# Optimization experiments

Measured on AMD Instinct MI355X. Metric: run time of the kernel, lower is better.

## Reference

```python
import jax, jax.numpy as jnp
import numpy as np

# ---- static config (from MACEConfig / MACELayerConfig) ----
N_NODES = 128
F_S = 128          # n_invariant_feat_hidden (0e channels)
F_V = 64           # n_vectors_hidden (1e channels)
N_BESSEL = 8       # bessel_number
R_MAX = 5.0        # r_max
N_LAYERS = 2       # n_interactions
HID_RAD = 64       # radial MLP hidden width
F_S_OUT = 128      # n_invariant_feat_readout
F_V_OUT = 64       # n_vectors_readout
AVG_NEIGH = float(N_NODES)  # avg_num_neighbors default = n_nodes
RAD_OUT = F_S + 3 * F_V     # per-edge radial channel weights for the 4 TP paths


def _senders_receivers(n):
    # fully connected graph, matching get_senders_and_receivers
    s = np.repeat(np.arange(n), n - 1)
    j = np.tile(np.arange(1, n), n)
    r = (s + j) % n
    return jnp.asarray(s, dtype=jnp.int32), jnp.asarray(r, dtype=jnp.int32)


def _bessel(r):
    # e3nn bessel basis: sqrt(2/c) sin(n pi r / c) / r, n = 1..N_BESSEL
    n = jnp.arange(1, N_BESSEL + 1, dtype=r.dtype)
    return jnp.sqrt(2.0 / R_MAX) * jnp.sin(n * jnp.pi * r[:, None] / R_MAX) / r[:, None]


def _envelope(r):
    # smooth radial cutoff (polynomial p=6), stand-in for e3nn soft_envelope
    u = r / R_MAX
    p = 6.0
    env = 1.0 - (p + 1) * (p + 2) / 2 * u ** p + p * (p + 2) * u ** (p + 1) - p * (p + 1) / 2 * u ** (p + 2)
    return jnp.where(u < 1.0, env, 0.0)


def _forward(x, species_embed, Wr1, Wr2, W_sv, W_mix_s, W_mix_v, W_out_s, W_out_v):
    senders, receivers = _senders_receivers(N_NODES)

    def single(pos):  # pos: (N, 3)
        com = pos.mean(axis=0)                       # centre of mass (3,)
        v = pos[receivers] - pos[senders]            # edge relative vectors (E, 3)
        r = jnp.linalg.norm(v, axis=-1) + 1e-8       # (E,)
        vhat = v / r[:, None]
        rb = _bessel(r) * _envelope(r)[:, None]      # (E, N_BESSEL)

        s = jnp.broadcast_to(species_embed[0], (N_NODES, F_S))       # 0e node feats
        V = jnp.zeros((N_NODES, F_V, 3), dtype=pos.dtype)            # 1e node feats

        for l in range(N_LAYERS):
            # learned per-edge radial weights for each tensor-product path
            h = jax.nn.silu(rb @ Wr1[l]) @ Wr2[l]    # (E, RAD_OUT)
            R0 = h[:, :F_S]
            R1 = h[:, F_S:F_S + F_V]
            R2 = h[:, F_S + F_V:F_S + 2 * F_V]
            R3 = h[:, F_S + 2 * F_V:]

            s_src = s[senders]                       # gather (E, F_S)
            V_src = V[senders]                       # gather (E, F_V, 3)

            # CG tensor-product paths (only 0e and 1e irreps present):
            m0a = R0 * s_src                                         # 0e x 0e -> 0e
            m0b = R1 * jnp.einsum('efk,ek->ef', V_src, vhat)         # 1e x 1e -> 0e
            m1a = (R2 * (s_src @ W_sv[l]))[..., None] * vhat[:, None, :]  # 0e x 1e -> 1e
            m1b = R3[..., None] * V_src                              # 1e x 0e -> 1e

            # scatter-sum message passing over receivers
            agg0 = jax.ops.segment_sum(jnp.concatenate([m0a, m0b], -1), receivers,
                                       num_segments=N_NODES) / AVG_NEIGH   # (N, F_S+F_V)
            agg1 = jax.ops.segment_sum(jnp.concatenate([m1a, m1b], 1), receivers,
                                       num_segments=N_NODES) / AVG_NEIGH   # (N, 2F_V, 3)

            s = s + jax.nn.silu(agg0 @ W_mix_s[l])
            V = V + jnp.einsum('nfk,fg->ngk', agg1, W_mix_v[l])

        out_s = s @ W_out_s                                          # (N, F_S_OUT)
        out_v = jnp.einsum('nfk,fg->ngk', V, W_out_v) + com          # (N, F_V_OUT, 3) + CoM
        return out_v, out_s

    return jax.vmap(single)(x)


def setup_inputs() -> dict:
    key = jax.random.key(0)
    ks = jax.random.split(key, 10)
    sc = lambda fan: 1.0 / np.sqrt(fan)
    inp = {
        'x': jax.random.normal(ks[0], (8, N_NODES, 3), dtype=jnp.float32),
        'species_embed': jax.random.normal(ks[1], (1, F_S), dtype=jnp.float32),
        'Wr1': jax.random.normal(ks[2], (N_LAYERS, N_BESSEL, HID_RAD), dtype=jnp.float32) * sc(N_BESSEL),
        'Wr2': jax.random.normal(ks[3], (N_LAYERS, HID_RAD, RAD_OUT), dtype=jnp.float32) * sc(HID_RAD),
        'W_sv': jax.random.normal(ks[4], (N_LAYERS, F_S, F_V), dtype=jnp.float32) * sc(F_S),
        'W_mix_s': jax.random.normal(ks[5], (N_LAYERS, F_S + F_V, F_S), dtype=jnp.float32) * sc(F_S + F_V),
        'W_mix_v': jax.random.normal(ks[6], (N_LAYERS, 2 * F_V, F_V), dtype=jnp.float32) * sc(2 * F_V),
        'W_out_s': jax.random.normal(ks[7], (F_S, F_S_OUT), dtype=jnp.float32) * sc(F_S),
        'W_out_v': jax.random.normal(ks[8], (F_V, F_V_OUT), dtype=jnp.float32) * sc(F_V),
    }
    return inp


def reference(x, species_embed, Wr1, Wr2, W_sv, W_mix_s, W_mix_v, W_out_s, W_out_v):
    return _forward(x, species_embed, Wr1, Wr2, W_sv, W_mix_s, W_mix_v, W_out_s, W_out_v)
```

## Files before the change

### kernel.cpp

```cpp
#include <hip/hip_runtime.h>
#include <math.h>

typedef unsigned short u16;
typedef __attribute__((ext_vector_type(8))) short frag_ab;
typedef __attribute__((ext_vector_type(4))) float frag_cd;

#define BATCH 8
#define NN 128
#define FS 128
#define FV 64
#define NB 8
#define HID 64
#define ROUT 320
#define HSTRB 72

#define SZ_S (BATCH*FS*NN)
#define SZ_V (BATCH*FV*3*NN)
#define SZ_T (BATCH*FV*NN)
#define N_W2B (ROUT*HID)
#define OFF_SB 0
#define OFF_VB (OFF_SB+SZ_S)
#define OFF_T1 (OFF_VB+SZ_V)
#define OFF_W2B (OFF_T1+SZ_T)

__device__ __forceinline__ float silu_f(float x){ return x * (1.0f/(1.0f + __expf(-x))); }

__device__ __forceinline__ u16 f2bf(float x){
  union { float f; unsigned int u; } v; v.f = x;
  unsigned int r = v.u + 0x7fffu + ((v.u >> 16) & 1u);
  return (u16)(r >> 16);
}
__device__ __forceinline__ float bf2f(u16 h){
  union { unsigned int u; float f; } v; v.u = ((unsigned int)h) << 16; return v.f;
}

__global__ __launch_bounds__(512) void layer0_kernel(
    const float* __restrict__ pos,
    const float* __restrict__ species,
    const float* __restrict__ Wr1l,
    const float* __restrict__ Wr2,
    const float* __restrict__ Wsv,
    const float* __restrict__ WmixSl,
    const float* __restrict__ WmixVl,
    float* __restrict__ sOut,
    float* __restrict__ vOut,
    float* __restrict__ tOut,
    u16*   __restrict__ w2b)
{
  const int tid = threadIdx.x;
  const int b   = blockIdx.x >> 6;
  const int k0  = (blockIdx.x & 63) * 2;

  __shared__ u16   hidB[2][128*HSTRB];
  __shared__ float vhx[2][128], vhy[2][128], vhz[2][128];
  __shared__ float colsum[2][4][64];
  __shared__ float aggS[2][128];
  __shared__ float dV[2][192];
  __shared__ float sNew[2][128];
  __shared__ float t0L[64];

  const float* pb   = pos + b*NN*3;
  const float* Wr2l = Wr2;

  {
    const int kk   = tid >> 8;
    const int r2   = tid & 255;
    const int i    = r2 & 127;
    const int half = r2 >> 7;
    const int k    = k0 + kk;
    float vx = pb[k*3+0]-pb[i*3+0];
    float vy = pb[k*3+1]-pb[i*3+1];
    float vz = pb[k*3+2]-pb[i*3+2];
    float r = sqrtf(vx*vx+vy*vy+vz*vz) + 1e-8f;
    float inv = 1.0f/r;
    if (half==0){ vhx[kk][i]=vx*inv; vhy[kk][i]=vy*inv; vhz[kk][i]=vz*inv; }
    float u = r*0.2f;
    float env = 0.0f;
    if (u < 1.0f && i != k){
      float u2=u*u, u6=u2*u2*u2;
      env = 1.0f - 28.0f*u6 + 48.0f*u6*u - 21.0f*u6*u2;
    }
    float coef = 0.6324555320336759f * inv * env;
    float th   = r * 0.6283185307179586f;
    float s1 = __sinf(th), c1 = __cosf(th);
    float rb[NB];
    rb[0] = coef*s1;
    float twoc = 2.f*c1, sp = s1, spp = 0.f;
    #pragma unroll
    for(int n=1;n<NB;n++){ float s = twoc*sp - spp; spp = sp; sp = s; rb[n] = coef*s; }
    u16* hrow = hidB[kk] + i*HSTRB;
    #pragma unroll
    for(int jg=0;jg<8;jg++){
      const int jgg = half*8 + jg;
      float h0=0.f,h1=0.f,h2=0.f,h3=0.f;
      #pragma unroll
      for(int n=0;n<NB;n++){
        const float* wr = Wr1l + n*HID + jgg*4;
        float rn = rb[n];
        h0 = fmaf(rn, wr[0], h0);
        h1 = fmaf(rn, wr[1], h1);
        h2 = fmaf(rn, wr[2], h2);
        h3 = fmaf(rn, wr[3], h3);
      }
      ushort4 uu = make_ushort4(f2bf(silu_f(h0)), f2bf(silu_f(h1)),
                                f2bf(silu_f(h2)), f2bf(silu_f(h3)));
      *(ushort4*)(hrow + jgg*4) = uu;
    }
  }
  __syncthreads();

  {
    const int kk  = tid >> 8;
    const int var = (tid >> 6) & 3;
    const int j   = tid & 63;
    const u16* hb = hidB[kk];
    float a0 = 0.f, a1 = 0.f;
    if (var == 0){
      #pragma unroll 8
      for (int i=0;i<128;i+=2){
        a0 += bf2f(hb[i*HSTRB + j]);
        a1 += bf2f(hb[(i+1)*HSTRB + j]);
      }
    } else {
      const float* wv = (var==1) ? vhx[kk] : (var==2) ? vhy[kk] : vhz[kk];
      #pragma unroll 8
      for (int i=0;i<128;i+=2){
        a0 = fmaf(bf2f(hb[i*HSTRB + j]),     wv[i],   a0);
        a1 = fmaf(bf2f(hb[(i+1)*HSTRB + j]), wv[i+1], a1);
      }
    }
    colsum[kk][var][j] = a0+a1;
  }
  __syncthreads();

  if (tid < 128){
    const int c = tid;
    float d00=0.f,d01=0.f, d10=0.f,d11=0.f;
    #pragma unroll 8
    for (int j=0;j<HID;j+=2){
      float w0 = Wr2l[j*ROUT + c];
      float w1 = Wr2l[(j+1)*ROUT + c];
      d00 = fmaf(colsum[0][0][j],   w0, d00);
      d01 = fmaf(colsum[0][0][j+1], w1, d01);
      d10 = fmaf(colsum[1][0][j],   w0, d10);
      d11 = fmaf(colsum[1][0][j+1], w1, d11);
    }
    float sc = species[c] * (1.0f/128.0f);
    aggS[0][c] = sc * (d00+d01);
    aggS[1][c] = sc * (d10+d11);
  } else if (tid < 320){
    const int o = tid - 128;
    const int f = o & 63, c3 = o >> 6;
    float d00=0.f,d01=0.f, d10=0.f,d11=0.f;
    #pragma unroll 8
    for (int j=0;j<HID;j+=2){
      float w0 = Wr2l[j*ROUT + 192 + f];
      float w1 = Wr2l[(j+1)*ROUT + 192 + f];
      d00 = fmaf(colsum[0][1+c3][j],   w0, d00);
      d01 = fmaf(colsum[0][1+c3][j+1], w1, d01);
      d10 = fmaf(colsum[1][1+c3][j],   w0, d10);
      d11 = fmaf(colsum[1][1+c3][j+1], w1, d11);
    }
    dV[0][f*3+c3] = (d00+d01) * (1.0f/128.0f);
    dV[1][f*3+c3] = (d10+d11) * (1.0f/128.0f);
  } else if (tid < 384){
    const int g = tid - 320;
    float a0=0.f, a1=0.f;
    #pragma unroll 8
    for (int c=0; c<FS; c+=2){
      a0 = fmaf(species[c],   Wsv[c*FV+g],     a0);
      a1 = fmaf(species[c+1], Wsv[(c+1)*FV+g], a1);
    }
    t0L[g] = a0+a1;
  } else if (tid < 424){
    const int t = blockIdx.x*40 + (tid-384);
    const int j = t & 63, c = t >> 6;
    w2b[t] = f2bf(Wr2[HID*ROUT + j*ROUT + c]);
  }
  __syncthreads();

  if (tid < FS){
    float a00=0.f,a01=0.f, a10=0.f,a11=0.f;
    #pragma unroll 8
    for (int cc=0; cc<128; cc+=2){
      float w0 = WmixSl[cc*FS+tid];
      float w1 = WmixSl[(cc+1)*FS+tid];
      a00 = fmaf(aggS[0][cc],   w0, a00);
      a01 = fmaf(aggS[0][cc+1], w1, a01);
      a10 = fmaf(aggS[1][cc],   w0, a10);
      a11 = fmaf(aggS[1][cc+1], w1, a11);
    }
    float sn0 = species[tid] + silu_f(a00+a01);
    float sn1 = species[tid] + silu_f(a10+a11);
    sNew[0][tid] = sn0;
    sNew[1][tid] = sn1;
    sOut[(b*FS+tid)*NN + k0]     = sn0;
    sOut[(b*FS+tid)*NN + k0 + 1] = sn1;
  } else if (tid < 320){
    const int o = tid - 128;
    const int g = o/3, c3 = o - g*3;
    float a0=0.f, a1=0.f;
    #pragma unroll 8
    for (int f=0; f<FV; f++){
      float w = WmixVl[f*FV+g];
      float tf = t0L[f];
      a0 = fmaf(tf*dV[0][f*3+c3], w, a0);
      a1 = fmaf(tf*dV[1][f*3+c3], w, a1);
    }
    vOut[(b*FV*3 + o)*NN + k0]     = a0;
    vOut[(b*FV*3 + o)*NN + k0 + 1] = a1;
  }
  __syncthreads();

  if (tid < FV){
    const float* Wsv1 = Wsv + FS*FV;
    float a00=0.f,a01=0.f, a10=0.f,a11=0.f;
    #pragma unroll 8
    for (int f=0; f<FS; f+=2){
      float w0 = Wsv1[f*FV+tid];
      float w1 = Wsv1[(f+1)*FV+tid];
      a00 = fmaf(sNew[0][f],   w0, a00);
      a01 = fmaf(sNew[0][f+1], w1, a01);
      a10 = fmaf(sNew[1][f],   w0, a10);
      a11 = fmaf(sNew[1][f+1], w1, a11);
    }
    tOut[(b*FV+tid)*NN + k0]     = (a00+a01);
    tOut[(b*FV+tid)*NN + k0 + 1] = (a10+a11);
  }
}

__global__ __launch_bounds__(1024) void layer_kernel(
    const float* __restrict__ pos,
    const float* __restrict__ sIn,
    const float* __restrict__ vIn,
    const float* __restrict__ tIn,
    const float* __restrict__ Wr1l,
    const u16*   __restrict__ w2bl,
    const float* __restrict__ WmixSl,
    const float* __restrict__ WmixVl,
    const float* __restrict__ WoutS,
    const float* __restrict__ WoutV,
    float* __restrict__ outp)
{
  const int tid  = threadIdx.x;
  const int b    = blockIdx.x >> 5;
  const int k0   = (blockIdx.x & 31) * 4;
  const int w    = tid >> 6;
  const int lane = tid & 63;
  const int col  = lane & 15;
  const int quad = lane >> 4;
  const int gh   = w & 1;
  const int wq   = (w >> 1) & 3;
  const int sh   = w >> 3;

  __shared__ u16   hidB[4][128*HSTRB];
  __shared__ float vhx[4][128], vhy[4][128], vhz[4][128];
  __shared__ float aggP[4][2][576];
  __shared__ float sPart[4][4][FS];
  __shared__ float sNew[4][FS];
  __shared__ float vNewL[4][192];
  __shared__ float comL[3];

  const float* pb = pos + b*NN*3;

  {
    const int jh = tid >> 9;
    const int kk = (tid >> 7) & 3;
    const int i  = tid & 127;
    const int k  = k0 + kk;
    float vx = pb[k*3+0]-pb[i*3+0];
    float vy = pb[k*3+1]-pb[i*3+1];
    float vz = pb[k*3+2]-pb[i*3+2];
    float r = sqrtf(vx*vx+vy*vy+vz*vz) + 1e-8f;
    float inv = 1.0f/r;
    if (jh == 0){ vhx[kk][i]=vx*inv; vhy[kk][i]=vy*inv; vhz[kk][i]=vz*inv; }
    float u = r*0.2f;
    float env = 0.0f;
    if (u < 1.0f && i != k){
      float u2=u*u, u6=u2*u2*u2;
      env = 1.0f - 28.0f*u6 + 48.0f*u6*u - 21.0f*u6*u2;
    }
    float coef = 0.6324555320336759f * inv * env;
    float th   = r * 0.6283185307179586f;
    float s1 = __sinf(th), c1 = __cosf(th);
    float rb[NB];
    rb[0] = coef*s1;
    float twoc = 2.f*c1, sp = s1, spp = 0.f;
    #pragma unroll
    for(int n=1;n<NB;n++){ float s = twoc*sp - spp; spp = sp; sp = s; rb[n] = coef*s; }
    u16* hrow = hidB[kk] + i*HSTRB;
    #pragma unroll
    for(int jg0=0;jg0<8;jg0++){
      const int jg = jh*8 + jg0;
      float h0=0.f,h1=0.f,h2=0.f,h3=0.f;
      #pragma unroll
      for(int n=0;n<NB;n++){
        const float* wr = Wr1l + n*HID + jg*4;
        float rn = rb[n];
        h0 = fmaf(rn, wr[0], h0);
        h1 = fmaf(rn, wr[1], h1);
        h2 = fmaf(rn, wr[2], h2);
        h3 = fmaf(rn, wr[3], h3);
      }
      ushort4 uu = make_ushort4(f2bf(silu_f(h0)), f2bf(silu_f(h1)),
                                f2bf(silu_f(h2)), f2bf(silu_f(h3)));
      *(ushort4*)(hrow + jg*4) = uu;
    }
    if (tid < 3){
      float a0=0.f, a1=0.f;
      for (int n=0;n<NN;n+=2){ a0 += pb[n*3+tid]; a1 += pb[(n+1)*3+tid]; }
      comL[tid] = (a0+a1) * (1.0f/128.0f);
    }
  }
  __syncthreads();

  const float* sIb = sIn + b*FS*NN;
  const float* vIb = vIn + b*FV*3*NN;
  const float* tIb = tIn + b*FV*NN;
  const int i00 = sh*64 + quad*4;

  if (gh == 0){
    const int c_s0 = wq*16 + col;
    const int c_s1 = 64 + c_s0;

    const u16* wp0 = w2bl + c_s0*HID + quad*8;
    const u16* wp1 = w2bl + c_s1*HID + quad*8;
    const u16* wp2 = w2bl + (128 + c_s0)*HID + quad*8;
    const frag_ab b00 = *(const frag_ab*)(wp0), b01 = *(const frag_ab*)(wp0+32);
    const frag_ab b10 = *(const frag_ab*)(wp1), b11 = *(const frag_ab*)(wp1+32);
    const frag_ab b20 = *(const frag_ab*)(wp2), b21 = *(const frag_ab*)(wp2+32);

    const float* fs0 = sIb + c_s0*NN + i00;
    const float* fs1 = sIb + c_s1*NN + i00;
    const float* fv  = vIb + c_s0*3*NN + i00;

    float sA0[4]={0.f,0.f,0.f,0.f}, sA1[4]={0.f,0.f,0.f,0.f}, sA2[4]={0.f,0.f,0.f,0.f};

    #pragma unroll 1
    for (int mt=0; mt<4; mt++){
      float4 s4a = *(const float4*)&fs0[mt*16];
      float4 s4b = *(const float4*)&fs1[mt*16];
      float4 vx4 = *(const float4*)&fv[mt*16];
      float4 vy4 = *(const float4*)&fv[NN + mt*16];
      float4 vz4 = *(const float4*)&fv[2*NN + mt*16];
      const int hbase = (sh*64 + mt*16 + col)*HSTRB + quad*8;
      const int vbase = i00 + mt*16;
      #pragma unroll
      for (int kk=0; kk<4; kk++){
        frag_ab a0 = *(const frag_ab*)&hidB[kk][hbase];
        frag_ab a1 = *(const frag_ab*)&hidB[kk][hbase + 32];
        float4 hx4 = *(const float4*)&vhx[kk][vbase];
        float4 hy4 = *(const float4*)&vhy[kk][vbase];
        float4 hz4 = *(const float4*)&vhz[kk][vbase];
        frag_cd ac0 = {0.f,0.f,0.f,0.f};
        frag_cd ac1 = {0.f,0.f,0.f,0.f};
        frag_cd ac2 = {0.f,0.f,0.f,0.f};
        ac0 = __builtin_amdgcn_mfma_f32_16x16x32_bf16(a0, b00, ac0, 0,0,0);
        ac1 = __builtin_amdgcn_mfma_f32_16x16x32_bf16(a0, b10, ac1, 0,0,0);
        ac2 = __builtin_amdgcn_mfma_f32_16x16x32_bf16(a0, b20, ac2, 0,0,0);
        ac0 = __builtin_amdgcn_mfma_f32_16x16x32_bf16(a1, b01, ac0, 0,0,0);
        ac1 = __builtin_amdgcn_mfma_f32_16x16x32_bf16(a1, b11, ac1, 0,0,0);
        ac2 = __builtin_amdgcn_mfma_f32_16x16x32_bf16(a1, b21, ac2, 0,0,0);

        sA0[kk] += ac0[0]*s4a.x + ac0[1]*s4a.y + ac0[2]*s4a.z + ac0[3]*s4a.w;
        sA1[kk] += ac1[0]*s4b.x + ac1[1]*s4b.y + ac1[2]*s4b.z + ac1[3]*s4b.w;
        sA2[kk] += ac2[0]*(vx4.x*hx4.x + vy4.x*hy4.x + vz4.x*hz4.x)
                 + ac2[1]*(vx4.y*hx4.y + vy4.y*hy4.y + vz4.y*hz4.y)
                 + ac2[2]*(vx4.z*hx4.z + vy4.z*hy4.z + vz4.z*hz4.z)
                 + ac2[3]*(vx4.w*hx4.w + vy4.w*hy4.w + vz4.w*hz4.w);
      }
    }
    #pragma unroll
    for (int kk=0; kk<4; kk++){
      float v0 = sA0[kk]; v0 += __shfl_xor(v0,16,64); v0 += __shfl_xor(v0,32,64);
      float v1 = sA1[kk]; v1 += __shfl_xor(v1,16,64); v1 += __shfl_xor(v1,32,64);
      float v2 = sA2[kk]; v2 += __shfl_xor(v2,16,64); v2 += __shfl_xor(v2,32,64);
      if (lane < 16){
        aggP[kk][sh][wq*16 + lane]       = v0;
        aggP[kk][sh][64 + wq*16 + lane]  = v1;
        aggP[kk][sh][128 + wq*16 + lane] = v2;
      }
    }
  } else {
    const int f_vc = wq*16 + col;

    const u16* wp3 = w2bl + (192 + f_vc)*HID + quad*8;
    const u16* wp4 = w2bl + (256 + f_vc)*HID + quad*8;
    const frag_ab b30 = *(const frag_ab*)(wp3), b31 = *(const frag_ab*)(wp3+32);
    const frag_ab b40 = *(const frag_ab*)(wp4), b41 = *(const frag_ab*)(wp4+32);

    const float* fv = vIb + f_vc*3*NN + i00;
    const float* ft = tIb + f_vc*NN + i00;

    float sX3[4]={0.f,0.f,0.f,0.f}, sY3[4]={0.f,0.f,0.f,0.f}, sZ3[4]={0.f,0.f,0.f,0.f};
    float sX4[4]={0.f,0.f,0.f,0.f}, sY4[4]={0.f,0.f,0.f,0.f}, sZ4[4]={0.f,0.f,0.f,0.f};

    #pragma unroll 1
    for (int mt=0; mt<4; mt++){
      float4 vx4 = *(const float4*)&fv[mt*16];
      float4 vy4 = *(const float4*)&fv[NN + mt*16];
      float4 vz4 = *(const float4*)&fv[2*NN + mt*16];
      float4 t4  = *(const float4*)&ft[mt*16];
      const int hbase = (sh*64 + mt*16 + col)*HSTRB + quad*8;
      const int vbase = i00 + mt*16;
      #pragma unroll
      for (int kk=0; kk<4; kk++){
        frag_ab a0 = *(const frag_ab*)&hidB[kk][hbase];
        frag_ab a1 = *(const frag_ab*)&hidB[kk][hbase + 32];
        float4 hx4 = *(const float4*)&vhx[kk][vbase];
        float4 hy4 = *(const float4*)&vhy[kk][vbase];
        float4 hz4 = *(const float4*)&vhz[kk][vbase];
        frag_cd ac3 = {0.f,0.f,0.f,0.f};
        frag_cd ac4 = {0.f,0.f,0.f,0.f};
        ac3 = __builtin_amdgcn_mfma_f32_16x16x32_bf16(a0, b30, ac3, 0,0,0);
        ac4 = __builtin_amdgcn_mfma_f32_16x16x32_bf16(a0, b40, ac4, 0,0,0);
        ac3 = __builtin_amdgcn_mfma_f32_16x16x32_bf16(a1, b31, ac3, 0,0,0);
        ac4 = __builtin_amdgcn_mfma_f32_16x16x32_bf16(a1, b41, ac4, 0,0,0);

        float t0_ = ac3[0]*t4.x, t1_ = ac3[1]*t4.y, t2_ = ac3[2]*t4.z, t3_ = ac3[3]*t4.w;
        sX3[kk] += t0_*hx4.x + t1_*hx4.y + t2_*hx4.z + t3_*hx4.w;
        sY3[kk] += t0_*hy4.x + t1_*hy4.y + t2_*hy4.z + t3_*hy4.w;
        sZ3[kk] += t0_*hz4.x + t1_*hz4.y + t2_*hz4.z + t3_*hz4.w;
        sX4[kk] += ac4[0]*vx4.x + ac4[1]*vx4.y + ac4[2]*vx4.z + ac4[3]*vx4.w;
        sY4[kk] += ac4[0]*vy4.x + ac4[1]*vy4.y + ac4[2]*vy4.z + ac4[3]*vy4.w;
        sZ4[kk] += ac4[0]*vz4.x + ac4[1]*vz4.y + ac4[2]*vz4.z + ac4[3]*vz4.w;
      }
    }
    #pragma unroll
    for (int kk=0; kk<4; kk++){
      float x3 = sX3[kk]; x3 += __shfl_xor(x3,16,64); x3 += __shfl_xor(x3,32,64);
      float y3 = sY3[kk]; y3 += __shfl_xor(y3,16,64); y3 += __shfl_xor(y3,32,64);
      float z3 = sZ3[kk]; z3 += __shfl_xor(z3,16,64); z3 += __shfl_xor(z3,32,64);
      float x4 = sX4[kk]; x4 += __shfl_xor(x4,16,64); x4 += __shfl_xor(x4,32,64);
      float y4 = sY4[kk]; y4 += __shfl_xor(y4,16,64); y4 += __shfl_xor(y4,32,64);
      float z4 = sZ4[kk]; z4 += __shfl_xor(z4,16,64); z4 += __shfl_xor(z4,32,64);
      if (lane < 16){
        const int f2 = wq*16 + lane;
        aggP[kk][sh][192+f2*3+0] = x3; aggP[kk][sh][192+f2*3+1] = y3; aggP[kk][sh][192+f2*3+2] = z3;
        aggP[kk][sh][384+f2*3+0] = x4; aggP[kk][sh][384+f2*3+1] = y4; aggP[kk][sh][384+f2*3+2] = z4;
      }
    }
  }

  __syncthreads();
  for (int t2=tid; t2<2304; t2+=1024){
    const int kk = t2 / 576;
    const int t  = t2 - kk*576;
    aggP[kk][0][t] = (aggP[kk][0][t] + aggP[kk][1][t]) * (1.0f/128.0f);
  }
  __syncthreads();

  if (tid < 512){
    const int o = tid & 127, p = tid >> 7;
    const int c0 = p*48;
    float a0=0.f,a1=0.f,a2=0.f,a3=0.f;
    #pragma unroll 8
    for (int cc=c0; cc<c0+48; cc++){
      float w0 = WmixSl[cc*FS+o];
      a0 = fmaf(aggP[0][0][cc], w0, a0);
      a1 = fmaf(aggP[1][0][cc], w0, a1);
      a2 = fmaf(aggP[2][0][cc], w0, a2);
      a3 = fmaf(aggP[3][0][cc], w0, a3);
    }
    sPart[0][p][o] = a0; sPart[1][p][o] = a1;
    sPart[2][p][o] = a2; sPart[3][p][o] = a3;
  } else if (tid < 704){
    const int o = tid - 512;
    const int g = o/3, c3 = o - g*3;
    float a0=0.f,a1=0.f,a2=0.f,a3=0.f;
    #pragma unroll 8
    for (int f=0; f<FV; f++){
      float w0 = WmixVl[f*FV+g];
      float w1 = WmixVl[(f+FV)*FV+g];
      a0 = fmaf(aggP[0][0][192+f*3+c3], w0, a0); a0 = fmaf(aggP[0][0][384+f*3+c3], w1, a0);
      a1 = fmaf(aggP[1][0][192+f*3+c3], w0, a1); a1 = fmaf(aggP[1][0][384+f*3+c3], w1, a1);
      a2 = fmaf(aggP[2][0][192+f*3+c3], w0, a2); a2 = fmaf(aggP[2][0][384+f*3+c3], w1, a2);
      a3 = fmaf(aggP[3][0][192+f*3+c3], w0, a3); a3 = fmaf(aggP[3][0][384+f*3+c3], w1, a3);
    }
    vNewL[0][o] = vIb[o*NN + k0]     + a0;
    vNewL[1][o] = vIb[o*NN + k0 + 1] + a1;
    vNewL[2][o] = vIb[o*NN + k0 + 2] + a2;
    vNewL[3][o] = vIb[o*NN + k0 + 3] + a3;
  }
  __syncthreads();

  if (tid < FS){
    #pragma unroll
    for (int kk=0; kk<4; kk++)
      sNew[kk][tid] = sIb[tid*NN + k0 + kk]
                    + silu_f(sPart[kk][0][tid] + sPart[kk][1][tid]
                           + sPart[kk][2][tid] + sPart[kk][3][tid]);
  } else if (tid < 320){
    const int o = tid - 128;
    const int g = o/3, c3 = o - g*3;
    float a0 = comL[c3], a1 = comL[c3], a2 = comL[c3], a3 = comL[c3];
    #pragma unroll 8
    for (int f=0; f<FV; f++){
      float wv = WoutV[f*FV+g];
      a0 = fmaf(vNewL[0][f*3+c3], wv, a0);
      a1 = fmaf(vNewL[1][f*3+c3], wv, a1);
      a2 = fmaf(vNewL[2][f*3+c3], wv, a2);
      a3 = fmaf(vNewL[3][f*3+c3], wv, a3);
    }
    outp[(b*NN+k0)*FV*3 + o]   = a0;
    outp[(b*NN+k0+1)*FV*3 + o] = a1;
    outp[(b*NN+k0+2)*FV*3 + o] = a2;
    outp[(b*NN+k0+3)*FV*3 + o] = a3;
  }
  __syncthreads();

  float* e3s = &aggP[0][0][0];
  if (tid < 512){
    const int o = tid & 127, p = tid >> 7;
    const int f0 = p*32;
    float a0=0.f,a1=0.f,a2=0.f,a3=0.f;
    #pragma unroll 8
    for (int f=f0; f<f0+32; f++){
      float w0 = WoutS[f*FS+o];
      a0 = fmaf(sNew[0][f], w0, a0);
      a1 = fmaf(sNew[1][f], w0, a1);
      a2 = fmaf(sNew[2][f], w0, a2);
      a3 = fmaf(sNew[3][f], w0, a3);
    }
    e3s[(p*4+0)*128 + o] = a0;
    e3s[(p*4+1)*128 + o] = a1;
    e3s[(p*4+2)*128 + o] = a2;
    e3s[(p*4+3)*128 + o] = a3;
  }
  __syncthreads();

  if (tid < 512){
    const int o = tid & 127, kk = tid >> 7;
    float a = e3s[(0*4+kk)*128 + o] + e3s[(1*4+kk)*128 + o]
            + e3s[(2*4+kk)*128 + o] + e3s[(3*4+kk)*128 + o];
    outp[BATCH*NN*FV*3 + (b*NN+k0+kk)*FS + o] = a;
  }
}

extern "C" void kernel_launch(void* const* d_in, const int* in_sizes, int n_in,
                              void* d_out, int out_size, void* d_ws, size_t ws_size,
                              hipStream_t stream)
{
  const float* x       = (const float*)d_in[0];
  const float* species = (const float*)d_in[1];
  const float* Wr1     = (const float*)d_in[2];
  const float* Wr2     = (const float*)d_in[3];
  const float* Wsv     = (const float*)d_in[4];
  const float* WmixS   = (const float*)d_in[5];
  const float* WmixV   = (const float*)d_in[6];
  const float* WoutS   = (const float*)d_in[7];
  const float* WoutV   = (const float*)d_in[8];
  float* ws  = (float*)d_ws;
  float* out = (float*)d_out;

  float* sB  = ws + OFF_SB;
  float* vB  = ws + OFF_VB;
  float* t1  = ws + OFF_T1;
  u16*   w2b = (u16*)(ws + OFF_W2B);

  layer0_kernel<<<BATCH*NN/2, 512, 0, stream>>>(x, species, Wr1, Wr2, Wsv,
      WmixS, WmixV, sB, vB, t1, w2b);

  layer_kernel<<<BATCH*NN/4, 1024, 0, stream>>>(x, sB, vB, t1,
      Wr1 + NB*HID, w2b, WmixS + 192*FS, WmixV + 128*FV,
      WoutS, WoutV, out);
}
```

Measured before the change: 126.0 us.

## Vectorise shared-memory reads with padded channel-major layouts and split t-projection

Rewrites the small per-node matvec loops in both kernels to read shared-memory operands as float4 instead of scalars. The vector aggregates dV, aggP and vNewL move from interleaved xyz to padded channel-major rows so those float4 reads are possible. The colsum reduction now loads two bf16 values per 32-bit read on half the threads, and the first kernel's t-projection is split across four thread groups with a shared-memory reduction. This cuts LDS instruction count and serial FMA depth, at the cost of an extra barrier and slightly more shared memory.

```diff
diff --git a/kernel.cpp b/kernel.cpp
--- a/kernel.cpp
+++ b/kernel.cpp
@@ -55,9 +55,10 @@
   __shared__ float vhx[2][128], vhy[2][128], vhz[2][128];
   __shared__ float colsum[2][4][64];
   __shared__ float aggS[2][128];
-  __shared__ float dV[2][192];
+  __shared__ float dV[2][204];
   __shared__ float sNew[2][128];
   __shared__ float t0L[64];
+  __shared__ float tPart[4][2][64];
 
   const float* pb   = pos + b*NN*3;
   const float* Wr2l = Wr2;
@@ -109,60 +110,72 @@
   }
   __syncthreads();
 
-  {
-    const int kk  = tid >> 8;
-    const int var = (tid >> 6) & 3;
-    const int j   = tid & 63;
-    const u16* hb = hidB[kk];
-    float a0 = 0.f, a1 = 0.f;
+  if (tid < 256){
+    const int kk = tid >> 7;
+    const int var = (tid >> 5) & 3;
+    const int jh  = tid & 31;
+    const u16* hb = hidB[kk] + 2*jh;
+    float a0=0.f,a1=0.f,c0_=0.f,c1_=0.f;
     if (var == 0){
       #pragma unroll 8
       for (int i=0;i<128;i+=2){
-        a0 += bf2f(hb[i*HSTRB + j]);
-        a1 += bf2f(hb[(i+1)*HSTRB + j]);
+        unsigned int v0 = *(const unsigned int*)(hb + i*HSTRB);
+        unsigned int v1 = *(const unsigned int*)(hb + (i+1)*HSTRB);
+        a0  += bf2f((u16)(v0 & 0xffffu)); a1  += bf2f((u16)(v0 >> 16));
+        c0_ += bf2f((u16)(v1 & 0xffffu)); c1_ += bf2f((u16)(v1 >> 16));
       }
     } else {
       const float* wv = (var==1) ? vhx[kk] : (var==2) ? vhy[kk] : vhz[kk];
       #pragma unroll 8
       for (int i=0;i<128;i+=2){
-        a0 = fmaf(bf2f(hb[i*HSTRB + j]),     wv[i],   a0);
-        a1 = fmaf(bf2f(hb[(i+1)*HSTRB + j]), wv[i+1], a1);
-      }
-    }
-    colsum[kk][var][j] = a0+a1;
+        unsigned int v0 = *(const unsigned int*)(hb + i*HSTRB);
+        unsigned int v1 = *(const unsigned int*)(hb + (i+1)*HSTRB);
+        float w0 = wv[i], w1 = wv[i+1];
+        a0  = fmaf(bf2f((u16)(v0 & 0xffffu)), w0, a0);
+        a1  = fmaf(bf2f((u16)(v0 >> 16)),     w0, a1);
+        c0_ = fmaf(bf2f((u16)(v1 & 0xffffu)), w1, c0_);
+        c1_ = fmaf(bf2f((u16)(v1 >> 16)),     w1, c1_);
+      }
+    }
+    colsum[kk][var][2*jh]   = a0+c0_;
+    colsum[kk][var][2*jh+1] = a1+c1_;
   }
   __syncthreads();
 
   if (tid < 128){
     const int c = tid;
-    float d00=0.f,d01=0.f, d10=0.f,d11=0.f;
-    #pragma unroll 8
-    for (int j=0;j<HID;j+=2){
-      float w0 = Wr2l[j*ROUT + c];
-      float w1 = Wr2l[(j+1)*ROUT + c];
-      d00 = fmaf(colsum[0][0][j],   w0, d00);
-      d01 = fmaf(colsum[0][0][j+1], w1, d01);
-      d10 = fmaf(colsum[1][0][j],   w0, d10);
-      d11 = fmaf(colsum[1][0][j+1], w1, d11);
+    float d0=0.f, d1=0.f;
+    #pragma unroll 2
+    for (int j0=0;j0<HID;j0+=4){
+      float4 s0 = *(const float4*)&colsum[0][0][j0];
+      float4 s1 = *(const float4*)&colsum[1][0][j0];
+      float w0 = Wr2l[j0*ROUT + c];
+      float w1 = Wr2l[(j0+1)*ROUT + c];
+      float w2 = Wr2l[(j0+2)*ROUT + c];
+      float w3 = Wr2l[(j0+3)*ROUT + c];
+      d0 = fmaf(s0.x,w0,d0); d0 = fmaf(s0.y,w1,d0); d0 = fmaf(s0.z,w2,d0); d0 = fmaf(s0.w,w3,d0);
+      d1 = fmaf(s1.x,w0,d1); d1 = fmaf(s1.y,w1,d1); d1 = fmaf(s1.z,w2,d1); d1 = fmaf(s1.w,w3,d1);
     }
     float sc = species[c] * (1.0f/128.0f);
-    aggS[0][c] = sc * (d00+d01);
-    aggS[1][c] = sc * (d10+d11);
+    aggS[0][c] = sc * d0;
+    aggS[1][c] = sc * d1;
   } else if (tid < 320){
     const int o = tid - 128;
     const int f = o & 63, c3 = o >> 6;
-    float d00=0.f,d01=0.f, d10=0.f,d11=0.f;
-    #pragma unroll 8
-    for (int j=0;j<HID;j+=2){
-      float w0 = Wr2l[j*ROUT + 192 + f];
-      float w1 = Wr2l[(j+1)*ROUT + 192 + f];
-      d00 = fmaf(colsum[0][1+c3][j],   w0, d00);
-      d01 = fmaf(colsum[0][1+c3][j+1], w1, d01);
-      d10 = fmaf(colsum[1][1+c3][j],   w0, d10);
-      d11 = fmaf(colsum[1][1+c3][j+1], w1, d11);
-    }
-    dV[0][f*3+c3] = (d00+d01) * (1.0f/128.0f);
-    dV[1][f*3+c3] = (d10+d11) * (1.0f/128.0f);
+    float d0=0.f, d1=0.f;
+    #pragma unroll 2
+    for (int j0=0;j0<HID;j0+=4){
+      float4 s0 = *(const float4*)&colsum[0][1+c3][j0];
+      float4 s1 = *(const float4*)&colsum[1][1+c3][j0];
+      float w0 = Wr2l[j0*ROUT + 192 + f];
+      float w1 = Wr2l[(j0+1)*ROUT + 192 + f];
+      float w2 = Wr2l[(j0+2)*ROUT + 192 + f];
+      float w3 = Wr2l[(j0+3)*ROUT + 192 + f];
+      d0 = fmaf(s0.x,w0,d0); d0 = fmaf(s0.y,w1,d0); d0 = fmaf(s0.z,w2,d0); d0 = fmaf(s0.w,w3,d0);
+      d1 = fmaf(s1.x,w0,d1); d1 = fmaf(s1.y,w1,d1); d1 = fmaf(s1.z,w2,d1); d1 = fmaf(s1.w,w3,d1);
+    }
+    dV[0][c3*68+f] = d0 * (1.0f/128.0f);
+    dV[1][c3*68+f] = d1 * (1.0f/128.0f);
   } else if (tid < 384){
     const int g = tid - 320;
     float a0=0.f, a1=0.f;
@@ -180,18 +193,20 @@
   __syncthreads();
 
   if (tid < FS){
-    float a00=0.f,a01=0.f, a10=0.f,a11=0.f;
-    #pragma unroll 8
-    for (int cc=0; cc<128; cc+=2){
-      float w0 = WmixSl[cc*FS+tid];
-      float w1 = WmixSl[(cc+1)*FS+tid];
-      a00 = fmaf(aggS[0][cc],   w0, a00);
-      a01 = fmaf(aggS[0][cc+1], w1, a01);
-      a10 = fmaf(aggS[1][cc],   w0, a10);
-      a11 = fmaf(aggS[1][cc+1], w1, a11);
-    }
-    float sn0 = species[tid] + silu_f(a00+a01);
-    float sn1 = species[tid] + silu_f(a10+a11);
+    float a0=0.f, a1=0.f;
+    #pragma unroll 2
+    for (int c0=0; c0<128; c0+=4){
+      float4 g0 = *(const float4*)&aggS[0][c0];
+      float4 g1 = *(const float4*)&aggS[1][c0];
+      float w0 = WmixSl[c0*FS+tid];
+      float w1 = WmixSl[(c0+1)*FS+tid];
+      float w2 = WmixSl[(c0+2)*FS+tid];
+      float w3 = WmixSl[(c0+3)*FS+tid];
+      a0 = fmaf(g0.x,w0,a0); a0 = fmaf(g0.y,w1,a0); a0 = fmaf(g0.z,w2,a0); a0 = fmaf(g0.w,w3,a0);
+      a1 = fmaf(g1.x,w0,a1); a1 = fmaf(g1.y,w1,a1); a1 = fmaf(g1.z,w2,a1); a1 = fmaf(g1.w,w3,a1);
+    }
+    float sn0 = species[tid] + silu_f(a0);
+    float sn1 = species[tid] + silu_f(a1);
     sNew[0][tid] = sn0;
     sNew[1][tid] = sn1;
     sOut[(b*FS+tid)*NN + k0]     = sn0;
@@ -200,32 +215,48 @@
     const int o = tid - 128;
     const int g = o/3, c3 = o - g*3;
     float a0=0.f, a1=0.f;
-    #pragma unroll 8
-    for (int f=0; f<FV; f++){
-      float w = WmixVl[f*FV+g];
-      float tf = t0L[f];
-      a0 = fmaf(tf*dV[0][f*3+c3], w, a0);
-      a1 = fmaf(tf*dV[1][f*3+c3], w, a1);
+    #pragma unroll 2
+    for (int f0=0; f0<FV; f0+=4){
+      float4 dv0 = *(const float4*)&dV[0][c3*68+f0];
+      float4 dv1 = *(const float4*)&dV[1][c3*68+f0];
+      float4 t4  = *(const float4*)&t0L[f0];
+      float w0 = WmixVl[f0*FV+g];
+      float w1 = WmixVl[(f0+1)*FV+g];
+      float w2 = WmixVl[(f0+2)*FV+g];
+      float w3 = WmixVl[(f0+3)*FV+g];
+      a0 = fmaf(t4.x*dv0.x, w0, a0); a0 = fmaf(t4.y*dv0.y, w1, a0);
+      a0 = fmaf(t4.z*dv0.z, w2, a0); a0 = fmaf(t4.w*dv0.w, w3, a0);
+      a1 = fmaf(t4.x*dv1.x, w0, a1); a1 = fmaf(t4.y*dv1.y, w1, a1);
+      a1 = fmaf(t4.z*dv1.z, w2, a1); a1 = fmaf(t4.w*dv1.w, w3, a1);
     }
     vOut[(b*FV*3 + o)*NN + k0]     = a0;
     vOut[(b*FV*3 + o)*NN + k0 + 1] = a1;
   }
   __syncthreads();
 
-  if (tid < FV){
+  if (tid < 256){
+    const int g = tid & 63, p = tid >> 6;
     const float* Wsv1 = Wsv + FS*FV;
-    float a00=0.f,a01=0.f, a10=0.f,a11=0.f;
-    #pragma unroll 8
-    for (int f=0; f<FS; f+=2){
-      float w0 = Wsv1[f*FV+tid];
-      float w1 = Wsv1[(f+1)*FV+tid];
-      a00 = fmaf(sNew[0][f],   w0, a00);
-      a01 = fmaf(sNew[0][f+1], w1, a01);
-      a10 = fmaf(sNew[1][f],   w0, a10);
-      a11 = fmaf(sNew[1][f+1], w1, a11);
-    }
-    tOut[(b*FV+tid)*NN + k0]     = (a00+a01);
-    tOut[(b*FV+tid)*NN + k0 + 1] = (a10+a11);
+    const int f0 = p*32;
+    float a0=0.f, a1=0.f;
+    #pragma unroll 2
+    for (int f=f0; f<f0+32; f+=4){
+      float4 s0 = *(const float4*)&sNew[0][f];
+      float4 s1 = *(const float4*)&sNew[1][f];
+      float w0 = Wsv1[f*FV+g];
+      float w1 = Wsv1[(f+1)*FV+g];
+      float w2 = Wsv1[(f+2)*FV+g];
+      float w3 = Wsv1[(f+3)*FV+g];
+      a0 = fmaf(s0.x,w0,a0); a0 = fmaf(s0.y,w1,a0); a0 = fmaf(s0.z,w2,a0); a0 = fmaf(s0.w,w3,a0);
+      a1 = fmaf(s1.x,w0,a1); a1 = fmaf(s1.y,w1,a1); a1 = fmaf(s1.z,w2,a1); a1 = fmaf(s1.w,w3,a1);
+    }
+    tPart[p][0][g] = a0; tPart[p][1][g] = a1;
+  }
+  __syncthreads();
+  if (tid < 128){
+    const int g = tid & 63, kk = tid >> 6;
+    tOut[(b*FV+g)*NN + k0 + kk] =
+        tPart[0][kk][g] + tPart[1][kk][g] + tPart[2][kk][g] + tPart[3][kk][g];
   }
 }
 
@@ -255,10 +286,10 @@
 
   __shared__ u16   hidB[4][128*HSTRB];
   __shared__ float vhx[4][128], vhy[4][128], vhz[4][128];
-  __shared__ float aggP[4][2][576];
+  __shared__ float aggP[4][2][600];
   __shared__ float sPart[4][4][FS];
   __shared__ float sNew[4][FS];
-  __shared__ float vNewL[4][192];
+  __shared__ float vNewL[4][204];
   __shared__ float comL[3];
 
   const float* pb = pos + b*NN*3;
@@ -436,16 +467,20 @@
       float z4 = sZ4[kk]; z4 += __shfl_xor(z4,16,64); z4 += __shfl_xor(z4,32,64);
       if (lane < 16){
         const int f2 = wq*16 + lane;
-        aggP[kk][sh][192+f2*3+0] = x3; aggP[kk][sh][192+f2*3+1] = y3; aggP[kk][sh][192+f2*3+2] = z3;
-        aggP[kk][sh][384+f2*3+0] = x4; aggP[kk][sh][384+f2*3+1] = y4; aggP[kk][sh][384+f2*3+2] = z4;
-      }
-    }
-  }
-
-  __syncthreads();
-  for (int t2=tid; t2<2304; t2+=1024){
-    const int kk = t2 / 576;
-    const int t  = t2 - kk*576;
+        aggP[kk][sh][192       + f2] = x3;
+        aggP[kk][sh][192 +  68 + f2] = y3;
+        aggP[kk][sh][192 + 136 + f2] = z3;
+        aggP[kk][sh][396       + f2] = x4;
+        aggP[kk][sh][396 +  68 + f2] = y4;
+        aggP[kk][sh][396 + 136 + f2] = z4;
+      }
+    }
+  }
+
+  __syncthreads();
+  for (int t2=tid; t2<2400; t2+=1024){
+    const int kk = t2 / 600;
+    const int t  = t2 - kk*600;
     aggP[kk][0][t] = (aggP[kk][0][t] + aggP[kk][1][t]) * (1.0f/128.0f);
   }
   __syncthreads();
@@ -454,33 +489,59 @@
     const int o = tid & 127, p = tid >> 7;
     const int c0 = p*48;
     float a0=0.f,a1=0.f,a2=0.f,a3=0.f;
-    #pragma unroll 8
-    for (int cc=c0; cc<c0+48; cc++){
+    #pragma unroll 2
+    for (int cc=c0; cc<c0+48; cc+=4){
+      float4 g0 = *(const float4*)&aggP[0][0][cc];
+      float4 g1 = *(const float4*)&aggP[1][0][cc];
+      float4 g2 = *(const float4*)&aggP[2][0][cc];
+      float4 g3 = *(const float4*)&aggP[3][0][cc];
       float w0 = WmixSl[cc*FS+o];
-      a0 = fmaf(aggP[0][0][cc], w0, a0);
-      a1 = fmaf(aggP[1][0][cc], w0, a1);
-      a2 = fmaf(aggP[2][0][cc], w0, a2);
-      a3 = fmaf(aggP[3][0][cc], w0, a3);
+      float w1 = WmixSl[(cc+1)*FS+o];
+      float w2 = WmixSl[(cc+2)*FS+o];
+      float w3 = WmixSl[(cc+3)*FS+o];
+      a0 = fmaf(g0.x,w0,a0); a0 = fmaf(g0.y,w1,a0); a0 = fmaf(g0.z,w2,a0); a0 = fmaf(g0.w,w3,a0);
+      a1 = fmaf(g1.x,w0,a1); a1 = fmaf(g1.y,w1,a1); a1 = fmaf(g1.z,w2,a1); a1 = fmaf(g1.w,w3,a1);
+      a2 = fmaf(g2.x,w0,a2); a2 = fmaf(g2.y,w1,a2); a2 = fmaf(g2.z,w2,a2); a2 = fmaf(g2.w,w3,a2);
+      a3 = fmaf(g3.x,w0,a3); a3 = fmaf(g3.y,w1,a3); a3 = fmaf(g3.z,w2,a3); a3 = fmaf(g3.w,w3,a3);
     }
     sPart[0][p][o] = a0; sPart[1][p][o] = a1;
     sPart[2][p][o] = a2; sPart[3][p][o] = a3;
   } else if (tid < 704){
     const int o = tid - 512;
-    const int g = o/3, c3 = o - g*3;
+    const int c3 = o >> 6, g = o & 63;
     float a0=0.f,a1=0.f,a2=0.f,a3=0.f;
-    #pragma unroll 8
-    for (int f=0; f<FV; f++){
-      float w0 = WmixVl[f*FV+g];
-      float w1 = WmixVl[(f+FV)*FV+g];
-      a0 = fmaf(aggP[0][0][192+f*3+c3], w0, a0); a0 = fmaf(aggP[0][0][384+f*3+c3], w1, a0);
-      a1 = fmaf(aggP[1][0][192+f*3+c3], w0, a1); a1 = fmaf(aggP[1][0][384+f*3+c3], w1, a1);
-      a2 = fmaf(aggP[2][0][192+f*3+c3], w0, a2); a2 = fmaf(aggP[2][0][384+f*3+c3], w1, a2);
-      a3 = fmaf(aggP[3][0][192+f*3+c3], w0, a3); a3 = fmaf(aggP[3][0][384+f*3+c3], w1, a3);
-    }
-    vNewL[0][o] = vIb[o*NN + k0]     + a0;
-    vNewL[1][o] = vIb[o*NN + k0 + 1] + a1;
-    vNewL[2][o] = vIb[o*NN + k0 + 2] + a2;
-    vNewL[3][o] = vIb[o*NN + k0 + 3] + a3;
+    #pragma unroll 1
+    for (int f0=0; f0<FV; f0+=4){
+      float4 p0 = *(const float4*)&aggP[0][0][192+c3*68+f0];
+      float4 q0 = *(const float4*)&aggP[0][0][396+c3*68+f0];
+      float4 p1 = *(const float4*)&aggP[1][0][192+c3*68+f0];
+      float4 q1 = *(const float4*)&aggP[1][0][396+c3*68+f0];
+      float4 p2 = *(const float4*)&aggP[2][0][192+c3*68+f0];
+      float4 q2 = *(const float4*)&aggP[2][0][396+c3*68+f0];
+      float4 p3 = *(const float4*)&aggP[3][0][192+c3*68+f0];
+      float4 q3 = *(const float4*)&aggP[3][0][396+c3*68+f0];
+      float w00 = WmixVl[f0*FV+g];
+      float w01 = WmixVl[(f0+1)*FV+g];
+      float w02 = WmixVl[(f0+2)*FV+g];
+      float w03 = WmixVl[(f0+3)*FV+g];
+      float w10 = WmixVl[(f0+FV)*FV+g];
+      float w11 = WmixVl[(f0+FV+1)*FV+g];
+      float w12 = WmixVl[(f0+FV+2)*FV+g];
+      float w13 = WmixVl[(f0+FV+3)*FV+g];
+      a0 = fmaf(p0.x,w00,a0); a0 = fmaf(p0.y,w01,a0); a0 = fmaf(p0.z,w02,a0); a0 = fmaf(p0.w,w03,a0);
+      a0 = fmaf(q0.x,w10,a0); a0 = fmaf(q0.y,w11,a0); a0 = fmaf(q0.z,w12,a0); a0 = fmaf(q0.w,w13,a0);
+      a1 = fmaf(p1.x,w00,a1); a1 = fmaf(p1.y,w01,a1); a1 = fmaf(p1.z,w02,a1); a1 = fmaf(p1.w,w03,a1);
+      a1 = fmaf(q1.x,w10,a1); a1 = fmaf(q1.y,w11,a1); a1 = fmaf(q1.z,w12,a1); a1 = fmaf(q1.w,w13,a1);
+      a2 = fmaf(p2.x,w00,a2); a2 = fmaf(p2.y,w01,a2); a2 = fmaf(p2.z,w02,a2); a2 = fmaf(p2.w,w03,a2);
+      a2 = fmaf(q2.x,w10,a2); a2 = fmaf(q2.y,w11,a2); a2 = fmaf(q2.z,w12,a2); a2 = fmaf(q2.w,w13,a2);
+      a3 = fmaf(p3.x,w00,a3); a3 = fmaf(p3.y,w01,a3); a3 = fmaf(p3.z,w02,a3); a3 = fmaf(p3.w,w03,a3);
+      a3 = fmaf(q3.x,w10,a3); a3 = fmaf(q3.y,w11,a3); a3 = fmaf(q3.z,w12,a3); a3 = fmaf(q3.w,w13,a3);
+    }
+    const int oo = g*3 + c3;
+    vNewL[0][c3*68+g] = vIb[oo*NN + k0]     + a0;
+    vNewL[1][c3*68+g] = vIb[oo*NN + k0 + 1] + a1;
+    vNewL[2][c3*68+g] = vIb[oo*NN + k0 + 2] + a2;
+    vNewL[3][c3*68+g] = vIb[oo*NN + k0 + 3] + a3;
   }
   __syncthreads();
 
@@ -494,13 +555,20 @@
     const int o = tid - 128;
     const int g = o/3, c3 = o - g*3;
     float a0 = comL[c3], a1 = comL[c3], a2 = comL[c3], a3 = comL[c3];
-    #pragma unroll 8
-    for (int f=0; f<FV; f++){
-      float wv = WoutV[f*FV+g];
-      a0 = fmaf(vNewL[0][f*3+c3], wv, a0);
-      a1 = fmaf(vNewL[1][f*3+c3], wv, a1);
-      a2 = fmaf(vNewL[2][f*3+c3], wv, a2);
-      a3 = fmaf(vNewL[3][f*3+c3], wv, a3);
+    #pragma unroll 2
+    for (int f0=0; f0<FV; f0+=4){
+      float4 v0 = *(const float4*)&vNewL[0][c3*68+f0];
+      float4 v1 = *(const float4*)&vNewL[1][c3*68+f0];
+      float4 v2 = *(const float4*)&vNewL[2][c3*68+f0];
+      float4 v3 = *(const float4*)&vNewL[3][c3*68+f0];
+      float w0 = WoutV[f0*FV+g];
+      float w1 = WoutV[(f0+1)*FV+g];
+      float w2 = WoutV[(f0+2)*FV+g];
+      float w3 = WoutV[(f0+3)*FV+g];
+      a0 = fmaf(v0.x,w0,a0); a0 = fmaf(v0.y,w1,a0); a0 = fmaf(v0.z,w2,a0); a0 = fmaf(v0.w,w3,a0);
+      a1 = fmaf(v1.x,w0,a1); a1 = fmaf(v1.y,w1,a1); a1 = fmaf(v1.z,w2,a1); a1 = fmaf(v1.w,w3,a1);
+      a2 = fmaf(v2.x,w0,a2); a2 = fmaf(v2.y,w1,a2); a2 = fmaf(v2.z,w2,a2); a2 = fmaf(v2.w,w3,a2);
+      a3 = fmaf(v3.x,w0,a3); a3 = fmaf(v3.y,w1,a3); a3 = fmaf(v3.z,w2,a3); a3 = fmaf(v3.w,w3,a3);
     }
     outp[(b*NN+k0)*FV*3 + o]   = a0;
     outp[(b*NN+k0+1)*FV*3 + o] = a1;
@@ -514,13 +582,20 @@
     const int o = tid & 127, p = tid >> 7;
     const int f0 = p*32;
     float a0=0.f,a1=0.f,a2=0.f,a3=0.f;
-    #pragma unroll 8
-    for (int f=f0; f<f0+32; f++){
+    #pragma unroll 2
+    for (int f=f0; f<f0+32; f+=4){
+      float4 s0 = *(const float4*)&sNew[0][f];
+      float4 s1 = *(const float4*)&sNew[1][f];
+      float4 s2 = *(const float4*)&sNew[2][f];
+      float4 s3 = *(const float4*)&sNew[3][f];
       float w0 = WoutS[f*FS+o];
-      a0 = fmaf(sNew[0][f], w0, a0);
-      a1 = fmaf(sNew[1][f], w0, a1);
-      a2 = fmaf(sNew[2][f], w0, a2);
-      a3 = fmaf(sNew[3][f], w0, a3);
+      float w1 = WoutS[(f+1)*FS+o];
+      float w2 = WoutS[(f+2)*FS+o];
+      float w3 = WoutS[(f+3)*FS+o];
+      a0 = fmaf(s0.x,w0,a0); a0 = fmaf(s0.y,w1,a0); a0 = fmaf(s0.z,w2,a0); a0 = fmaf(s0.w,w3,a0);
+      a1 = fmaf(s1.x,w0,a1); a1 = fmaf(s1.y,w1,a1); a1 = fmaf(s1.z,w2,a1); a1 = fmaf(s1.w,w3,a1);
+      a2 = fmaf(s2.x,w0,a2); a2 = fmaf(s2.y,w1,a2); a2 = fmaf(s2.z,w2,a2); a2 = fmaf(s2.w,w3,a2);
+      a3 = fmaf(s3.x,w0,a3); a3 = fmaf(s3.y,w1,a3); a3 = fmaf(s3.z,w2,a3); a3 = fmaf(s3.w,w3,a3);
     }
     e3s[(p*4+0)*128 + o] = a0;
     e3s[(p*4+1)*128 + o] = a1;
```

New measurement: 126.2 us. Within noise of the previous version (+0.2%).
